# Optimization experiments

Measured on AMD Instinct MI355X. Metric: run time of the kernel, lower is better.

## Reference

```python
import jax, jax.numpy as jnp
import numpy as np

EPS = 1e-5
TOP_N = 8
NUM_POINTS = 100
OUT_LO, OUT_HI = 0.0, 1.0


def setup_inputs() -> dict:
    key = jax.random.key(0)
    ks = jax.random.split(key, 7)
    B, D, M, R, MO = 2048, 8, 7, 32768, 9
    x = jax.random.normal(ks[0], (B, D), dtype=jnp.float32)
    # antecedent MF index per (rule, input); -1 means input unused in that rule
    antecedents = jax.random.randint(ks[1], (R, D), 0, M + 1) - 1  # values in [-1, M)
    consequents = jax.random.randint(ks[2], (R,), 0, MO)
    in_centers = jax.random.normal(ks[3], (D, M), dtype=jnp.float32)
    in_widths = 0.2 + 0.3 * jax.random.uniform(ks[4], (D, M), dtype=jnp.float32)
    out_centers = jax.random.uniform(ks[5], (MO,), dtype=jnp.float32)
    out_widths = 0.05 + 0.2 * jax.random.uniform(ks[6], (MO,), dtype=jnp.float32)
    return {"x": x, "antecedents": antecedents, "consequents": consequents,
            "in_centers": in_centers, "in_widths": in_widths,
            "out_centers": out_centers, "out_widths": out_widths}


def reference(x, antecedents, consequents, in_centers, in_widths, out_centers, out_widths):
    B, D = x.shape
    R = antecedents.shape[0]
    M = in_centers.shape[1]

    # Fuzzification: Gaussian input MFs, clamped like the torch module. mu: [B, D, M]
    z = (x[:, :, None] - in_centers[None, :, :]) / in_widths[None, :, :]
    mu = jnp.clip(jnp.exp(-0.5 * z * z), EPS, 1.0)

    # Rule firing strengths: product over inputs of selected memberships ([B, R]).
    # Small fixed loop over D (8) keeps peak memory at one [B, R] temp per step.
    firing = jnp.ones((B, R), dtype=x.dtype)
    for i in range(D):
        idx = antecedents[:, i]                      # [R], -1 => unused
        safe = jnp.clip(idx, 0, M - 1)
        vals = mu[:, i, safe]                        # [B, R]
        firing = firing * jnp.where(idx[None, :] == -1, jnp.ones((), x.dtype), vals)

    top_vals, top_idx = jax.lax.top_k(firing, TOP_N)  # [B, TOP_N]

    # Output universe and output MF table: [MO, P]
    universe = jnp.linspace(OUT_LO, OUT_HI, NUM_POINTS, dtype=x.dtype)
    zo = (universe[None, :] - out_centers[:, None]) / out_widths[:, None]
    out_mu = jnp.exp(-0.5 * zo * zo)

    # Mamdani implication (product) + aggregation (sum) + centroid defuzzification
    cons_top = consequents[top_idx]                   # [B, TOP_N]
    implications = top_vals[:, :, None] * out_mu[cons_top]  # [B, TOP_N, P]
    aggregated = implications.sum(axis=1)             # [B, P]
    numerator = (universe[None, :] * aggregated).sum(axis=1)
    denominator = aggregated.sum(axis=1) + EPS
    return numerator / denominator
```

## Files before the change

### kernel.cpp

```cpp
#include <hip/hip_runtime.h>
#include <math.h>

#define DD 8
#define MM 7
#define MOO 9
#define NPTS 100
#define EPSF 1e-5f

#define THREADS 1024
#define ITERS 8
#define ROWS 8
#define CAP 256
#define THR_SLACK 0.9879f

typedef unsigned uint32x4 __attribute__((ext_vector_type(4)));

__device__ __forceinline__ float bl(unsigned u) { return __uint_as_float(u << 16); }
__device__ __forceinline__ float bh(unsigned u) { return __uint_as_float(u & 0xFFFF0000u); }
__device__ __forceinline__ unsigned pkb(float a, float b) {
    return (__float_as_uint(b) & 0xFFFF0000u) | (__float_as_uint(a) >> 16);
}

__global__ __launch_bounds__(256) void pack_kernel(const int* __restrict__ ant,
                                                   unsigned* __restrict__ g_off,
                                                   int R) {
    int r = blockIdx.x * 256 + threadIdx.x;
    if (r < R) {
        const int4* a = reinterpret_cast<const int4*>(ant) + (size_t)r * 2;
        int4 lo = a[0], hi = a[1];
        int v[8] = {lo.x, lo.y, lo.z, lo.w, hi.x, hi.y, hi.z, hi.w};
        unsigned code = 0u;
        #pragma unroll
        for (int i = 0; i < 8; ++i) {
            int c = v[i];
            c = (c < 0) ? 7 : (c > MM - 1 ? MM - 1 : c);
            code |= (unsigned)c << (3 * i);
        }
        g_off[r] = (code & 4095u) | (((code >> 12) + 4096u) << 16);
    }
}

__global__ __launch_bounds__(THREADS, 4) void anfis_fused8(
    const float* __restrict__ x,
    const unsigned* __restrict__ stream_off,
    const int* __restrict__ consequents,
    const float* __restrict__ in_centers,
    const float* __restrict__ in_widths,
    const float* __restrict__ out_centers,
    const float* __restrict__ out_widths,
    float* __restrict__ out)
{
    __shared__ uint4 quads[8192];
    __shared__ float mu[ROWS][64];
    __shared__ float pairs[ROWS][256];
    __shared__ uint4 smaxpk[THREADS];
    __shared__ float s0s[MOO], s1s[MOO];
    __shared__ float sT[ROWS];
    __shared__ int   scnt[ROWS];
    __shared__ int   wlcnt;
    __shared__ float wv[ROWS][8];
    __shared__ int   wc[ROWS][8];

    const int tid = threadIdx.x;
    const int b0  = blockIdx.x * ROWS;

    unsigned short* wl = (unsigned short*)quads;
    float* cvals = (float*)(quads + 1024);
    int*   cidx  = (int*)(quads + 1536);

    if (tid < 512) {
        int row = tid >> 6, d = (tid >> 3) & 7, c = tid & 7;
        float v = 1.0f;
        if (c < MM) {
            float z = (x[(b0 + row) * DD + d] - in_centers[d * MM + c]) / in_widths[d * MM + c];
            v = expf(-0.5f * z * z);
            v = fminf(v, 1.0f);
            v = fmaxf(v, EPSF);
        }
        mu[row][(d << 3) + c] = v;
    } else if (tid >= 544 && tid < 544 + ROWS) {
        scnt[tid - 544] = 0;
    } else if (tid == 560) {
        wlcnt = 0;
    }
    __syncthreads();

    #pragma unroll
    for (int i = 0; i < 2; ++i) {
        int k = tid + i * THREADS;
        int row = k >> 8, e = k & 255;
        int p = e >> 6, q = e & 63;
        pairs[row][e] = mu[row][(2 * p) * 8 + (q & 7)] * mu[row][(2 * p + 1) * 8 + (q >> 3)];
    }
    __syncthreads();

    #pragma unroll
    for (int h = 0; h < 2; ++h) {
        float a8[ROWS];
        const int ia = h * 128 + (tid & 63);
        #pragma unroll
        for (int r = 0; r < ROWS; ++r) a8[r] = pairs[r][ia];
        #pragma unroll
        for (int ii = 0; ii < 4; ++ii) {
            int k = tid + (h * 4 + ii) * THREADS;
            int ib = h * 128 + 64 + ((((tid >> 6) + 16 * ii)) & 63);
            float q0 = a8[0] * pairs[0][ib];
            float q1 = a8[1] * pairs[1][ib];
            float q2 = a8[2] * pairs[2][ib];
            float q3 = a8[3] * pairs[3][ib];
            float q4 = a8[4] * pairs[4][ib];
            float q5 = a8[5] * pairs[5][ib];
            float q6 = a8[6] * pairs[6][ib];
            float q7 = a8[7] * pairs[7][ib];
            quads[k] = make_uint4(pkb(q0, q1), pkb(q2, q3), pkb(q4, q5), pkb(q6, q7));
        }
    }
    __syncthreads();

    const uint4* pk4 = reinterpret_cast<const uint4*>(stream_off);
    const unsigned qbase = (unsigned)(uintptr_t)&quads[0];
    float m[ROWS];
    #pragma unroll
    for (int r = 0; r < ROWS; ++r) m[r] = -1.0f;
    {
        uint32x4 a0, a1, a2, a3, b0, b1, b2, b3;
        uint32x4 c0, c1, c2, c3, d0, d1, d2, d3;

        #define ISSUE(J, RA0, RB0, RA1, RB1, RA2, RB2, RA3, RB3)                   \
        {                                                                          \
            uint4 cd = pk4[(J) * THREADS + tid];                                   \
            asm volatile("ds_read_b128 %0, %1" : "=v"(RA0) : "v"(qbase + ((cd.x & 0xFFFFu) << 4))); \
            asm volatile("ds_read_b128 %0, %1" : "=v"(RB0) : "v"(qbase + ((cd.x >> 16) << 4)));     \
            asm volatile("ds_read_b128 %0, %1" : "=v"(RA1) : "v"(qbase + ((cd.y & 0xFFFFu) << 4))); \
            asm volatile("ds_read_b128 %0, %1" : "=v"(RB1) : "v"(qbase + ((cd.y >> 16) << 4)));     \
            asm volatile("ds_read_b128 %0, %1" : "=v"(RA2) : "v"(qbase + ((cd.z & 0xFFFFu) << 4))); \
            asm volatile("ds_read_b128 %0, %1" : "=v"(RB2) : "v"(qbase + ((cd.z >> 16) << 4)));     \
            asm volatile("ds_read_b128 %0, %1" : "=v"(RA3) : "v"(qbase + ((cd.w & 0xFFFFu) << 4))); \
            asm volatile("ds_read_b128 %0, %1" : "=v"(RB3) : "v"(qbase + ((cd.w >> 16) << 4)));     \
        }
        #define RULE8(A, B)                                                        \
            m[0] = fmaxf(m[0], bl((A)[0]) * bl((B)[0]));                           \
            m[1] = fmaxf(m[1], bh((A)[0]) * bh((B)[0]));                           \
            m[2] = fmaxf(m[2], bl((A)[1]) * bl((B)[1]));                           \
            m[3] = fmaxf(m[3], bh((A)[1]) * bh((B)[1]));                           \
            m[4] = fmaxf(m[4], bl((A)[2]) * bl((B)[2]));                           \
            m[5] = fmaxf(m[5], bh((A)[2]) * bh((B)[2]));                           \
            m[6] = fmaxf(m[6], bl((A)[3]) * bl((B)[3]));                           \
            m[7] = fmaxf(m[7], bh((A)[3]) * bh((B)[3]));
        #define WAIT8()                                                            \
            __builtin_amdgcn_sched_barrier(0);                                     \
            asm volatile("s_waitcnt lgkmcnt(8)" ::: "memory");                     \
            __builtin_amdgcn_sched_barrier(0);
        #define WAIT0()                                                            \
            __builtin_amdgcn_sched_barrier(0);                                     \
            asm volatile("s_waitcnt lgkmcnt(0)" ::: "memory");                     \
            __builtin_amdgcn_sched_barrier(0);
        #define CONA  RULE8(a0, b0) RULE8(a1, b1) RULE8(a2, b2) RULE8(a3, b3)
        #define CONB  RULE8(c0, d0) RULE8(c1, d1) RULE8(c2, d2) RULE8(c3, d3)

        ISSUE(0, a0, b0, a1, b1, a2, b2, a3, b3)
        ISSUE(1, c0, d0, c1, d1, c2, d2, c3, d3)  WAIT8()  CONA
        ISSUE(2, a0, b0, a1, b1, a2, b2, a3, b3)  WAIT8()  CONB
        ISSUE(3, c0, d0, c1, d1, c2, d2, c3, d3)  WAIT8()  CONA
        ISSUE(4, a0, b0, a1, b1, a2, b2, a3, b3)  WAIT8()  CONB
        ISSUE(5, c0, d0, c1, d1, c2, d2, c3, d3)  WAIT8()  CONA
        ISSUE(6, a0, b0, a1, b1, a2, b2, a3, b3)  WAIT8()  CONB
        ISSUE(7, c0, d0, c1, d1, c2, d2, c3, d3)  WAIT8()  CONA
        WAIT0()  CONB

        #undef ISSUE
        #undef RULE8
        #undef WAIT8
        #undef WAIT0
        #undef CONA
        #undef CONB
    }
    smaxpk[tid] = make_uint4(pkb(m[0], m[1]), pkb(m[2], m[3]),
                             pkb(m[4], m[5]), pkb(m[6], m[7]));
    __syncthreads();

    if (tid < 512) {
        int row = tid >> 6, lane = tid & 63;
        float mm[16];
        #pragma unroll
        for (int k = 0; k < 16; ++k) {
            uint4 e = smaxpk[lane + 64 * k];
            unsigned word = (row & 4) ? ((row & 2) ? e.w : e.z)
                                      : ((row & 2) ? e.y : e.x);
            mm[k] = (row & 1) ? bh(word) : bl(word);
        }
        float thr = -1.0f;
        #pragma unroll
        for (int round = 0; round < 8; ++round) {
            float lm = mm[0];
            #pragma unroll
            for (int k = 1; k < 16; ++k) lm = fmaxf(lm, mm[k]);
            float wm = lm;
            #pragma unroll
            for (int off = 32; off >= 1; off >>= 1)
                wm = fmaxf(wm, __shfl_xor(wm, off, 64));
            unsigned long long bal = __ballot(lm == wm);
            int first = (int)__ffsll(bal) - 1;
            if (lane == first) {
                bool done = false;
                #pragma unroll
                for (int k = 0; k < 16; ++k) {
                    bool rm = (!done) && (mm[k] == wm);
                    mm[k] = rm ? -2.0f : mm[k];
                    done = done || rm;
                }
            }
            thr = wm;
        }
        if (lane == 0) sT[row] = thr;
    } else if (tid < 512 + MOO) {
        int mo = tid - 512;
        float oc = out_centers[mo], ow = out_widths[mo];
        float s0 = 0.0f, s1 = 0.0f;
        for (int p = 0; p < NPTS; ++p) {
            float u = (float)p * (1.0f / 99.0f);
            float z = (u - oc) / ow;
            float e = expf(-0.5f * z * z);
            s0 += e;
            s1 += u * e;
        }
        s0s[mo] = s0;
        s1s[mo] = s1;
    }
    __syncthreads();

    {
        const int lane = tid & 63;
        #pragma unroll
        for (int row = 0; row < ROWS; ++row) {
            bool q = m[row] >= THR_SLACK * sT[row];
            unsigned long long bal = __ballot(q);
            if (bal) {
                int lead = (int)__ffsll(bal) - 1;
                int base = 0;
                if (lane == lead) base = atomicAdd(&wlcnt, (int)__popcll(bal));
                base = __shfl(base, lead, 64);
                if (q) {
                    int off = (int)__popcll(bal & ((1ull << lane) - 1ull));
                    wl[base + off] = (unsigned short)((row << 10) | tid);
                }
            }
        }
    }
    __syncthreads();

    {
        const int hl = tid & 31;
        const int j = hl >> 2, s = hl & 3;
        const int n = wlcnt;
        for (int i = (tid >> 5); i < n; i += 32) {
            int it  = wl[i];
            int row = it >> 10;
            int t   = it & 1023;
            int flat = (j * THREADS + t) * 4 + s;
            unsigned w = stream_off[flat];
            unsigned lo12 = w & 0xFFFFu;
            unsigned hi12 = (w >> 16) - 4096u;
            const float* P = pairs[row];
            float f = (P[lo12 & 63u] * P[64 + (lo12 >> 6)])
                    * (P[128 + (hi12 & 63u)] * P[192 + (hi12 >> 6)]);
            if (f >= sT[row]) {
                int pos = atomicAdd(&scnt[row], 1);
                if (pos < CAP) {
                    cvals[row * CAP + pos] = f;
                    cidx[row * CAP + pos]  = flat;
                }
            }
        }
    }
    __syncthreads();

    if (tid < 512) {
        int row = tid >> 6, lane = tid & 63;
        int n = scnt[row] < CAP ? scnt[row] : CAP;
        for (int c = lane; c < n; c += 64) {
            float v  = cvals[row * CAP + c];
            int   id = cidx[row * CAP + c];
            int rk = 0;
            for (int mI = 0; mI < n; ++mI) {
                float vm = cvals[row * CAP + mI];
                int   im = cidx[row * CAP + mI];
                rk += ((vm > v) || (vm == v && im < id)) ? 1 : 0;
            }
            if (rk < 8) {
                wv[row][rk] = v;
                wc[row][rk] = consequents[id];
            }
        }
    }
    __syncthreads();

    if (tid < ROWS) {
        int row = tid;
        float num = 0.0f, den = 0.0f;
        #pragma unroll
        for (int k = 0; k < 8; ++k) {
            num += wv[row][k] * s1s[wc[row][k]];
            den += wv[row][k] * s0s[wc[row][k]];
        }
        out[b0 + row] = num / (den + EPSF);
    }
}

__global__ __launch_bounds__(256) void anfis_kernel(
    const float* __restrict__ x,
    const int* __restrict__ ant,
    const int* __restrict__ consequents,
    const float* __restrict__ in_centers,
    const float* __restrict__ in_widths,
    const float* __restrict__ out_centers,
    const float* __restrict__ out_widths,
    float* __restrict__ out,
    int R)
{
    __shared__ float mu[64];
    __shared__ float pairs[256];
    __shared__ float s0s[MOO], s1s[MOO];
    __shared__ float svals[256][9];
    __shared__ int   sidx[256][9];

    const int tid = threadIdx.x;
    const int b   = blockIdx.x;

    if (tid < 64) {
        int d = tid >> 3, c = tid & 7;
        float v = 1.0f;
        if (c < MM) {
            float z = (x[b * DD + d] - in_centers[d * MM + c]) / in_widths[d * MM + c];
            v = expf(-0.5f * z * z);
            v = fminf(v, 1.0f);
            v = fmaxf(v, EPSF);
        }
        mu[tid] = v;
    } else if (tid < 64 + MOO) {
        int mo = tid - 64;
        float oc = out_centers[mo], ow = out_widths[mo];
        float s0 = 0.0f, s1 = 0.0f;
        for (int p = 0; p < NPTS; ++p) {
            float u = (float)p * (1.0f / 99.0f);
            float z = (u - oc) / ow;
            float e = expf(-0.5f * z * z);
            s0 += e;
            s1 += u * e;
        }
        s0s[mo] = s0;
        s1s[mo] = s1;
    }
    __syncthreads();

    {
        int p = tid >> 6, q = tid & 63;
        pairs[tid] = mu[(2 * p) * 8 + (q & 7)] * mu[(2 * p + 1) * 8 + (q >> 3)];
    }
    __syncthreads();

    float vals[8];
    int   idxs[8];
    #pragma unroll
    for (int k = 0; k < 8; ++k) { vals[k] = -1.0f; idxs[k] = 0x7fffffff; }

    for (int r = tid; r < R; r += 256) {
        const int4* a = reinterpret_cast<const int4*>(ant) + (size_t)r * 2;
        int4 lo = a[0], hi = a[1];
        int v[8] = {lo.x, lo.y, lo.z, lo.w, hi.x, hi.y, hi.z, hi.w};
        unsigned code = 0u;
        #pragma unroll
        for (int i = 0; i < 8; ++i) {
            int c = v[i];
            c = (c < 0) ? 7 : (c > MM - 1 ? MM - 1 : c);
            code |= (unsigned)c << (3 * i);
        }
        float f = pairs[code & 63]
                * pairs[64  + ((code >> 6)  & 63)]
                * pairs[128 + ((code >> 12) & 63)]
                * pairs[192 + ((code >> 18) & 63)];
        if (f > vals[7]) {
            float nv = f; int ni = r;
            #pragma unroll
            for (int k = 0; k < 8; ++k) {
                bool take = nv > vals[k];
                float cv = vals[k]; int ci = idxs[k];
                vals[k] = take ? nv : cv;
                idxs[k] = take ? ni : ci;
                nv = take ? cv : nv;
                ni = take ? ci : ni;
            }
        }
    }

    #pragma unroll
    for (int k = 0; k < 8; ++k) { svals[tid][k] = vals[k]; sidx[tid][k] = idxs[k]; }

    for (int off = 128; off >= 1; off >>= 1) {
        __syncthreads();
        if (tid < off) {
            float ov[8]; int oi[8];
            int pa = 0, pb = 0;
            #pragma unroll
            for (int k = 0; k < 8; ++k) {
                float va = svals[tid][pa];        int ia = sidx[tid][pa];
                float vb = svals[tid + off][pb];  int ib = sidx[tid + off][pb];
                bool ta = (va > vb) || ((va == vb) && (ia < ib));
                ov[k] = ta ? va : vb;
                oi[k] = ta ? ia : ib;
                pa += ta ? 1 : 0;
                pb += ta ? 0 : 1;
            }
            #pragma unroll
            for (int k = 0; k < 8; ++k) { svals[tid][k] = ov[k]; sidx[tid][k] = oi[k]; }
        }
    }
    __syncthreads();

    if (tid == 0) {
        float num = 0.0f, den = 0.0f;
        #pragma unroll
        for (int k = 0; k < 8; ++k) {
            float v = svals[0][k];
            int   c = consequents[sidx[0][k]];
            num += v * s1s[c];
            den += v * s0s[c];
        }
        out[b] = num / (den + EPSF);
    }
}

extern "C" void kernel_launch(void* const* d_in, const int* in_sizes, int n_in,
                              void* d_out, int out_size, void* d_ws, size_t ws_size,
                              hipStream_t stream) {
    const float* x      = (const float*)d_in[0];
    const int*   ant    = (const int*)d_in[1];
    const int*   cons   = (const int*)d_in[2];
    const float* in_c   = (const float*)d_in[3];
    const float* in_w   = (const float*)d_in[4];
    const float* out_c  = (const float*)d_in[5];
    const float* out_w  = (const float*)d_in[6];
    float*       out    = (float*)d_out;

    const int B = in_sizes[0] / DD;
    const int R = in_sizes[1] / DD;

    const bool shape_ok = (R == THREADS * 4 * ITERS) && (B % ROWS == 0);
    const size_t need = (size_t)R * 4;

    if (shape_ok && d_ws && ws_size >= need) {
        unsigned* g_off = (unsigned*)d_ws;
        pack_kernel<<<(R + 255) / 256, 256, 0, stream>>>(ant, g_off, R);
        anfis_fused8<<<B / ROWS, THREADS, 0, stream>>>(x, g_off, cons, in_c, in_w,
                                                       out_c, out_w, out);
    } else {
        anfis_kernel<<<B, 256, 0, stream>>>(x, ant, cons, in_c, in_w,
                                            out_c, out_w, out, R);
    }
}
```

Before: 33.20 us.

## Replace bf16 product-max scan with packed int16 log-domain add/max

Quad products are now stored as quantized fixed-point log2 values in int16, so the hot rule scan uses packed integer add and max (v_pk_add_i16/v_pk_max_i16) instead of unpacking bf16 and doing float multiplies and maxes. The top-k threshold search runs on the integers, candidate pre-filtering uses a fixed log-domain slack, and the exact float recheck uses a converted threshold. The pairs table is also transposed to row-interleaved layout. This cuts VALU work in the dominant loop, but adds log computation in quad construction and relies on quantization plus slack to keep the true top-8 among the candidates.

New measurement: 34.10 us. 1.03x slower.

```diff
diff --git a/kernel.cpp b/kernel.cpp
--- a/kernel.cpp
+++ b/kernel.cpp
@@ -11,15 +11,9 @@
 #define ITERS 8
 #define ROWS 8
 #define CAP 256
-#define THR_SLACK 0.9879f
+#define LSLACK 6
 
 typedef unsigned uint32x4 __attribute__((ext_vector_type(4)));
-
-__device__ __forceinline__ float bl(unsigned u) { return __uint_as_float(u << 16); }
-__device__ __forceinline__ float bh(unsigned u) { return __uint_as_float(u & 0xFFFF0000u); }
-__device__ __forceinline__ unsigned pkb(float a, float b) {
-    return (__float_as_uint(b) & 0xFFFF0000u) | (__float_as_uint(a) >> 16);
-}
 
 __global__ __launch_bounds__(256) void pack_kernel(const int* __restrict__ ant,
                                                    unsigned* __restrict__ g_off,
@@ -52,10 +46,11 @@
 {
     __shared__ uint4 quads[8192];
     __shared__ float mu[ROWS][64];
-    __shared__ float pairs[ROWS][256];
+    __shared__ float pairs_t[2048];
     __shared__ uint4 smaxpk[THREADS];
     __shared__ float s0s[MOO], s1s[MOO];
-    __shared__ float sT[ROWS];
+    __shared__ int   sTi[ROWS];
+    __shared__ float sTf[ROWS];
     __shared__ int   scnt[ROWS];
     __shared__ int   wlcnt;
     __shared__ float wv[ROWS][8];
@@ -88,9 +83,9 @@
     #pragma unroll
     for (int i = 0; i < 2; ++i) {
         int k = tid + i * THREADS;
-        int row = k >> 8, e = k & 255;
+        int e = k >> 3, row = k & 7;
         int p = e >> 6, q = e & 63;
-        pairs[row][e] = mu[row][(2 * p) * 8 + (q & 7)] * mu[row][(2 * p + 1) * 8 + (q >> 3)];
+        pairs_t[k] = mu[row][(2 * p) * 8 + (q & 7)] * mu[row][(2 * p + 1) * 8 + (q >> 3)];
     }
     __syncthreads();
 
@@ -99,29 +94,29 @@
         float a8[ROWS];
         const int ia = h * 128 + (tid & 63);
         #pragma unroll
-        for (int r = 0; r < ROWS; ++r) a8[r] = pairs[r][ia];
+        for (int r = 0; r < ROWS; ++r) a8[r] = pairs_t[ia * 8 + r];
         #pragma unroll
         for (int ii = 0; ii < 4; ++ii) {
             int k = tid + (h * 4 + ii) * THREADS;
             int ib = h * 128 + 64 + ((((tid >> 6) + 16 * ii)) & 63);
-            float q0 = a8[0] * pairs[0][ib];
-            float q1 = a8[1] * pairs[1][ib];
-            float q2 = a8[2] * pairs[2][ib];
-            float q3 = a8[3] * pairs[3][ib];
-            float q4 = a8[4] * pairs[4][ib];
-            float q5 = a8[5] * pairs[5][ib];
-            float q6 = a8[6] * pairs[6][ib];
-            float q7 = a8[7] * pairs[7][ib];
-            quads[k] = make_uint4(pkb(q0, q1), pkb(q2, q3), pkb(q4, q5), pkb(q6, q7));
+            int l[ROWS];
+            #pragma unroll
+            for (int r = 0; r < ROWS; ++r) {
+                float q = a8[r] * pairs_t[ib * 8 + r];
+                l[r] = (int)floorf(__log2f(q) * 128.0f) - 1;
+            }
+            quads[k] = make_uint4(((unsigned)l[1] << 16) | ((unsigned)l[0] & 0xFFFFu),
+                                  ((unsigned)l[3] << 16) | ((unsigned)l[2] & 0xFFFFu),
+                                  ((unsigned)l[5] << 16) | ((unsigned)l[4] & 0xFFFFu),
+                                  ((unsigned)l[7] << 16) | ((unsigned)l[6] & 0xFFFFu));
         }
     }
     __syncthreads();
 
     const uint4* pk4 = reinterpret_cast<const uint4*>(stream_off);
     const unsigned qbase = (unsigned)(uintptr_t)&quads[0];
-    float m[ROWS];
-    #pragma unroll
-    for (int r = 0; r < ROWS; ++r) m[r] = -1.0f;
+    unsigned m01 = 0x80008000u, m23 = 0x80008000u;
+    unsigned m45 = 0x80008000u, m67 = 0x80008000u;
     {
         uint32x4 a0, a1, a2, a3, b0, b1, b2, b3;
         uint32x4 c0, c1, c2, c3, d0, d1, d2, d3;
@@ -138,15 +133,18 @@
             asm volatile("ds_read_b128 %0, %1" : "=v"(RA3) : "v"(qbase + ((cd.w & 0xFFFFu) << 4))); \
             asm volatile("ds_read_b128 %0, %1" : "=v"(RB3) : "v"(qbase + ((cd.w >> 16) << 4)));     \
         }
-        #define RULE8(A, B)                                                        \
-            m[0] = fmaxf(m[0], bl((A)[0]) * bl((B)[0]));                           \
-            m[1] = fmaxf(m[1], bh((A)[0]) * bh((B)[0]));                           \
-            m[2] = fmaxf(m[2], bl((A)[1]) * bl((B)[1]));                           \
-            m[3] = fmaxf(m[3], bh((A)[1]) * bh((B)[1]));                           \
-            m[4] = fmaxf(m[4], bl((A)[2]) * bl((B)[2]));                           \
-            m[5] = fmaxf(m[5], bh((A)[2]) * bh((B)[2]));                           \
-            m[6] = fmaxf(m[6], bl((A)[3]) * bl((B)[3]));                           \
-            m[7] = fmaxf(m[7], bh((A)[3]) * bh((B)[3]));
+        #define RULEPK(A, B)                                                       \
+        {                                                                          \
+            unsigned s0_, s1_, s2_, s3_;                                           \
+            asm("v_pk_add_i16 %0, %1, %2" : "=v"(s0_) : "v"((A)[0]), "v"((B)[0])); \
+            asm("v_pk_add_i16 %0, %1, %2" : "=v"(s1_) : "v"((A)[1]), "v"((B)[1])); \
+            asm("v_pk_add_i16 %0, %1, %2" : "=v"(s2_) : "v"((A)[2]), "v"((B)[2])); \
+            asm("v_pk_add_i16 %0, %1, %2" : "=v"(s3_) : "v"((A)[3]), "v"((B)[3])); \
+            asm("v_pk_max_i16 %0, %1, %2" : "=v"(m01) : "v"(m01), "v"(s0_));       \
+            asm("v_pk_max_i16 %0, %1, %2" : "=v"(m23) : "v"(m23), "v"(s1_));       \
+            asm("v_pk_max_i16 %0, %1, %2" : "=v"(m45) : "v"(m45), "v"(s2_));       \
+            asm("v_pk_max_i16 %0, %1, %2" : "=v"(m67) : "v"(m67), "v"(s3_));       \
+        }
         #define WAIT8()                                                            \
             __builtin_amdgcn_sched_barrier(0);                                     \
             asm volatile("s_waitcnt lgkmcnt(8)" ::: "memory");                     \
@@ -155,8 +153,8 @@
             __builtin_amdgcn_sched_barrier(0);                                     \
             asm volatile("s_waitcnt lgkmcnt(0)" ::: "memory");                     \
             __builtin_amdgcn_sched_barrier(0);
-        #define CONA  RULE8(a0, b0) RULE8(a1, b1) RULE8(a2, b2) RULE8(a3, b3)
-        #define CONB  RULE8(c0, d0) RULE8(c1, d1) RULE8(c2, d2) RULE8(c3, d3)
+        #define CONA  RULEPK(a0, b0) RULEPK(a1, b1) RULEPK(a2, b2) RULEPK(a3, b3)
+        #define CONB  RULEPK(c0, d0) RULEPK(c1, d1) RULEPK(c2, d2) RULEPK(c3, d3)
 
         ISSUE(0, a0, b0, a1, b1, a2, b2, a3, b3)
         ISSUE(1, c0, d0, c1, d1, c2, d2, c3, d3)  WAIT8()  CONA
@@ -169,36 +167,35 @@
         WAIT0()  CONB
 
         #undef ISSUE
-        #undef RULE8
+        #undef RULEPK
         #undef WAIT8
         #undef WAIT0
         #undef CONA
         #undef CONB
     }
-    smaxpk[tid] = make_uint4(pkb(m[0], m[1]), pkb(m[2], m[3]),
-                             pkb(m[4], m[5]), pkb(m[6], m[7]));
+    smaxpk[tid] = make_uint4(m01, m23, m45, m67);
     __syncthreads();
 
     if (tid < 512) {
         int row = tid >> 6, lane = tid & 63;
-        float mm[16];
+        int mm[16];
         #pragma unroll
         for (int k = 0; k < 16; ++k) {
             uint4 e = smaxpk[lane + 64 * k];
             unsigned word = (row & 4) ? ((row & 2) ? e.w : e.z)
                                       : ((row & 2) ? e.y : e.x);
-            mm[k] = (row & 1) ? bh(word) : bl(word);
-        }
-        float thr = -1.0f;
+            mm[k] = (row & 1) ? ((int)word >> 16) : ((int)(word << 16) >> 16);
+        }
+        int thr = -0x7FFFFFFF;
         #pragma unroll
         for (int round = 0; round < 8; ++round) {
-            float lm = mm[0];
-            #pragma unroll
-            for (int k = 1; k < 16; ++k) lm = fmaxf(lm, mm[k]);
-            float wm = lm;
+            int lm = mm[0];
+            #pragma unroll
+            for (int k = 1; k < 16; ++k) lm = max(lm, mm[k]);
+            int wm = lm;
             #pragma unroll
             for (int off = 32; off >= 1; off >>= 1)
-                wm = fmaxf(wm, __shfl_xor(wm, off, 64));
+                wm = max(wm, __shfl_xor(wm, off, 64));
             unsigned long long bal = __ballot(lm == wm);
             int first = (int)__ffsll(bal) - 1;
             if (lane == first) {
@@ -206,13 +203,16 @@
                 #pragma unroll
                 for (int k = 0; k < 16; ++k) {
                     bool rm = (!done) && (mm[k] == wm);
-                    mm[k] = rm ? -2.0f : mm[k];
+                    mm[k] = rm ? -0x7FFFFFFF : mm[k];
                     done = done || rm;
                 }
             }
             thr = wm;
         }
-        if (lane == 0) sT[row] = thr;
+        if (lane == 0) {
+            sTi[row] = thr;
+            sTf[row] = exp2f((float)thr * (1.0f / 128.0f)) * 0.9999f;
+        }
     } else if (tid < 512 + MOO) {
         int mo = tid - 512;
         float oc = out_centers[mo], ow = out_widths[mo];
@@ -231,9 +231,14 @@
 
     {
         const int lane = tid & 63;
+        int myl[8];
+        myl[0] = (int)(m01 << 16) >> 16;  myl[1] = (int)m01 >> 16;
+        myl[2] = (int)(m23 << 16) >> 16;  myl[3] = (int)m23 >> 16;
+        myl[4] = (int)(m45 << 16) >> 16;  myl[5] = (int)m45 >> 16;
+        myl[6] = (int)(m67 << 16) >> 16;  myl[7] = (int)m67 >> 16;
         #pragma unroll
         for (int row = 0; row < ROWS; ++row) {
-            bool q = m[row] >= THR_SLACK * sT[row];
+            bool q = myl[row] >= sTi[row] - LSLACK;
             unsigned long long bal = __ballot(q);
             if (bal) {
                 int lead = (int)__ffsll(bal) - 1;
@@ -261,10 +266,9 @@
             unsigned w = stream_off[flat];
             unsigned lo12 = w & 0xFFFFu;
             unsigned hi12 = (w >> 16) - 4096u;
-            const float* P = pairs[row];
-            float f = (P[lo12 & 63u] * P[64 + (lo12 >> 6)])
-                    * (P[128 + (hi12 & 63u)] * P[192 + (hi12 >> 6)]);
-            if (f >= sT[row]) {
+            float f = (pairs_t[(lo12 & 63u) * 8 + row] * pairs_t[(64 + (lo12 >> 6)) * 8 + row])
+                    * (pairs_t[(128 + (hi12 & 63u)) * 8 + row] * pairs_t[(192 + (hi12 >> 6)) * 8 + row]);
+            if (f >= sTf[row]) {
                 int pos = atomicAdd(&scnt[row], 1);
                 if (pos < CAP) {
                     cvals[row * CAP + pos] = f;
```
